# Optimization experiments

Hardware: AMD Instinct MI355X
Metric: run time of the kernel (lower is better)

## Reference

```python
import jax, jax.numpy as jnp
import numpy as np

B, N_ATOMS = 8192, 64      # molecules, atoms per molecule
DIM, EXTRA, N_CLS = 70, 7, 11
N_FP = 10000               # fingerprint vocab


def setup_inputs() -> dict:
    key = jax.random.key(0)
    ks = jax.random.split(key, 9)
    atoms = jax.random.randint(ks[0], (B, N_ATOMS), 0, N_FP, dtype=jnp.int64 if jax.config.jax_enable_x64 else jnp.int32)
    adjacency = jax.random.uniform(ks[1], (B, N_ATOMS, N_ATOMS), dtype=jnp.float32)
    sel_desc = jax.random.normal(ks[2], (B, EXTRA), dtype=jnp.float32)
    embed_table = jax.random.normal(ks[3], (N_FP, DIM), dtype=jnp.float32)
    w1 = jax.random.normal(ks[4], (DIM, DIM), dtype=jnp.float32) * 0.05
    b1 = jax.random.normal(ks[5], (DIM,), dtype=jnp.float32) * 0.05
    w2 = jax.random.normal(ks[6], (DIM, DIM), dtype=jnp.float32) * 0.05
    b2 = jax.random.normal(ks[7], (DIM,), dtype=jnp.float32) * 0.05
    wp = jax.random.normal(ks[8], (DIM + EXTRA, N_CLS), dtype=jnp.float32) * 0.05
    bp = jnp.zeros((N_CLS,), dtype=jnp.float32)
    return {"atoms": atoms, "adjacency": adjacency, "sel_desc": sel_desc,
            "embed_table": embed_table, "w1": w1, "b1": b1,
            "w2": w2, "b2": b2, "wp": wp, "bp": bp}


def reference(atoms, adjacency, sel_desc, embed_table, w1, b1, w2, b2, wp, bp):
    # embed atoms: [B, n, dim]
    x = embed_table[atoms]
    # message-passing layers: relu(linear) then (block-diagonal == batched) adjacency matmul
    for w, b in ((w1, b1), (w2, b2)):
        h = jax.nn.relu(jnp.einsum('bnd,de->bne', x, w) + b)
        x = jnp.einsum('bnm,bmd->bnd', adjacency, h)
    # segment-sum pool over atoms per molecule (sum_axis)
    y = jnp.sum(x, axis=1)                       # [B, dim]
    y = jnp.concatenate([y, sel_desc], axis=1)   # [B, dim+extra]
    return jnp.einsum('bd,dc->bc', y, wp) + bp   # [B, 11]
```

## Files before the change

kernel.cpp:

```cpp
#include <hip/hip_runtime.h>
#include <hip/hip_bf16.h>

#define NFP   10000
#define DIM   70
#define DPAD  72
#define NATOMS 64

typedef short  short8  __attribute__((ext_vector_type(8)));
typedef float  floatx4 __attribute__((ext_vector_type(4)));

__device__ inline unsigned short f2bf(float f) {
  union { float f; unsigned u; } x; x.f = f;
  unsigned r = x.u + 0x7fffu + ((x.u >> 16) & 1u);
  return (unsigned short)(r >> 16);
}

__device__ inline ushort2 pk2bf(float a, float b) {
  __hip_bfloat162 h = __float22bfloat162_rn(make_float2(a, b));
  union { __hip_bfloat162 h; ushort2 u; } c; c.h = h; return c.u;
}

__global__ __launch_bounds__(256) void precompute_G(
    const float* __restrict__ emb, const float* __restrict__ w1,
    const float* __restrict__ b1,  const float* __restrict__ w2,
    unsigned short* __restrict__ G) {
  __shared__ float w1s[DIM * DPAD];
  __shared__ float w2s[DIM * DPAD];
  __shared__ float b1s[DPAD];
  __shared__ float embs[32 * DPAD];
  __shared__ float e1s[32 * DPAD];
  const int t = threadIdx.x;

  for (int i = t; i < DIM * DPAD; i += 256) {
    int r = i / DPAD, c = i % DPAD;
    float v1 = 0.f, v2 = 0.f;
    if (c < DIM) { v1 = w1[r * DIM + c]; v2 = w2[r * DIM + c]; }
    w1s[i] = v1; w2s[i] = v2;
  }
  if (t < DPAD) b1s[t] = (t < DIM) ? b1[t] : 0.f;
  const int row0 = blockIdx.x * 32;
  for (int i = t; i < 32 * DPAD; i += 256) {
    int r = i / DPAD, c = i % DPAD;
    int vr = row0 + r;
    embs[i] = (vr < NFP && c < DIM) ? emb[vr * DIM + c] : 0.f;
  }
  __syncthreads();

  for (int task = t; task < 32 * 18; task += 256) {
    int r = task / 18, c4 = (task % 18) * 4;
    float4 acc = *(const float4*)&b1s[c4];
    for (int k = 0; k < DIM; k++) {
      float e = embs[r * DPAD + k];
      float4 w = *(const float4*)&w1s[k * DPAD + c4];
      acc.x = fmaf(e, w.x, acc.x); acc.y = fmaf(e, w.y, acc.y);
      acc.z = fmaf(e, w.z, acc.z); acc.w = fmaf(e, w.w, acc.w);
    }
    acc.x = fmaxf(acc.x, 0.f); acc.y = fmaxf(acc.y, 0.f);
    acc.z = fmaxf(acc.z, 0.f); acc.w = fmaxf(acc.w, 0.f);
    *(float4*)&e1s[r * DPAD + c4] = acc;
  }
  __syncthreads();

  for (int task = t; task < 32 * 18; task += 256) {
    int r = task / 18, c4 = (task % 18) * 4;
    int vr = row0 + r;
    if (vr >= NFP) continue;
    float ax = 0.f, ay = 0.f, az = 0.f, aw = 0.f;
    for (int k = 0; k < DIM; k++) {
      float e = e1s[r * DPAD + k];
      float4 w = *(const float4*)&w2s[k * DPAD + c4];
      ax = fmaf(e, w.x, ax); ay = fmaf(e, w.y, ay);
      az = fmaf(e, w.z, az); aw = fmaf(e, w.w, aw);
    }
    unsigned short* gp = G + vr * DPAD + c4;
    gp[0] = f2bf(ax); gp[1] = f2bf(ay); gp[2] = f2bf(az); gp[3] = f2bf(aw);
  }
}

__global__ __launch_bounds__(256) void mol_fused(
    const int* __restrict__ atoms, const float* __restrict__ adj,
    const float* __restrict__ b2,  const unsigned short* __restrict__ G,
    float* __restrict__ yws) {
  __shared__ unsigned short adjs[64 * DPAD];
  __shared__ unsigned short gTs[80 * DPAD];
  __shared__ float cwave[4 * 64];
  __shared__ float cvec[64];
  __shared__ float b2p[80];
  __shared__ float yacc[4 * 80];
  __shared__ int   satoms[64];

  const int b = blockIdx.x;
  const int t = threadIdx.x;
  const int w = t >> 6, lane = t & 63;
  const int q = lane >> 4, li = lane & 15;

  if (t < 64) satoms[t] = atoms[b * 64 + t];
  if (t < 80) b2p[t] = (t < DIM) ? b2[t] : 0.f;
  __syncthreads();

  {
    const float* ap = adj + (size_t)b * 4096;
    const int mc = (t & 15) * 4;
    const int a  = t >> 4;
    float4 cs = make_float4(0.f, 0.f, 0.f, 0.f);
#pragma unroll
    for (int it = 0; it < 4; it++) {
      int n = a + 16 * it;
      float4 v = *(const float4*)(ap + n * 64 + mc);
      cs.x += v.x; cs.y += v.y; cs.z += v.z; cs.w += v.w;
      ushort2 lo = pk2bf(v.x, v.y);
      ushort2 hi = pk2bf(v.z, v.w);
      ushort4 u; u.x = lo.x; u.y = lo.y; u.z = hi.x; u.w = hi.y;
      *(ushort4*)&adjs[n * DPAD + mc] = u;
    }
#pragma unroll
    for (int s = 16; s <= 32; s <<= 1) {
      cs.x += __shfl_xor(cs.x, s); cs.y += __shfl_xor(cs.y, s);
      cs.z += __shfl_xor(cs.z, s); cs.w += __shfl_xor(cs.w, s);
    }
    if (((t >> 4) & 3) == 0) *(float4*)&cwave[w * 64 + mc] = cs;
  }

  {
    const int m = t & 63;
    const int row = satoms[m];
    const uint4* Gv = (const uint4*)G;
    for (int ch = w; ch < 9; ch += 4) {
      uint4 v = Gv[row * 9 + ch];
      unsigned short* gp = &gTs[(ch * 8) * DPAD + m];
      gp[0 * DPAD] = (unsigned short)(v.x & 0xffff);
      gp[1 * DPAD] = (unsigned short)(v.x >> 16);
      gp[2 * DPAD] = (unsigned short)(v.y & 0xffff);
      gp[3 * DPAD] = (unsigned short)(v.y >> 16);
      gp[4 * DPAD] = (unsigned short)(v.z & 0xffff);
      gp[5 * DPAD] = (unsigned short)(v.z >> 16);
      gp[6 * DPAD] = (unsigned short)(v.w & 0xffff);
      gp[7 * DPAD] = (unsigned short)(v.w >> 16);
    }
    for (int i = t; i < 8 * DPAD; i += 256) gTs[72 * DPAD + i] = 0;
  }
  __syncthreads();

  if (t < 64) {
    cvec[t] = cwave[t] + cwave[64 + t] + cwave[128 + t] + cwave[192 + t];
  }

  const int R = w * 16;
  short8 a0 = *(const short8*)&adjs[(R + li) * DPAD + q * 8];
  short8 a1 = *(const short8*)&adjs[(R + li) * DPAD + 32 + q * 8];
  floatx4 acc[5];
#pragma unroll
  for (int nt = 0; nt < 5; nt++) {
    floatx4 z = {0.f, 0.f, 0.f, 0.f};
    short8 b0 = *(const short8*)&gTs[(nt * 16 + li) * DPAD + q * 8];
    short8 b1 = *(const short8*)&gTs[(nt * 16 + li) * DPAD + 32 + q * 8];
    z = __builtin_amdgcn_mfma_f32_16x16x32_bf16(a0, b0, z, 0, 0, 0);
    z = __builtin_amdgcn_mfma_f32_16x16x32_bf16(a1, b1, z, 0, 0, 0);
    acc[nt] = z;
  }
  __syncthreads();

  float ps[5];
#pragma unroll
  for (int nt = 0; nt < 5; nt++) {
    int d = nt * 16 + li;
    float bb = b2p[d];
    float p = 0.f;
#pragma unroll
    for (int r = 0; r < 4; r++) {
      float h = fmaxf(acc[nt][r] + bb, 0.f);
      p = fmaf(cvec[R + q * 4 + r], h, p);
    }
    p += __shfl_xor(p, 16);
    p += __shfl_xor(p, 32);
    ps[nt] = p;
  }
  if (q == 0) {
#pragma unroll
    for (int nt = 0; nt < 5; nt++) yacc[w * 80 + nt * 16 + li] = ps[nt];
  }
  __syncthreads();

  if (t < DIM) {
    float s = yacc[t] + yacc[80 + t] + yacc[160 + t] + yacc[240 + t];
    yws[(size_t)b * DIM + t] = s;
  }
}

__global__ __launch_bounds__(256) void proj_out(
    const float* __restrict__ yws, const float* __restrict__ sel,
    const float* __restrict__ wp,  const float* __restrict__ bp,
    float* __restrict__ out, int B) {
  __shared__ float wps[77 * 11];
  __shared__ float bps[11];
  const int t = threadIdx.x;
  for (int i = t; i < 77 * 11; i += 256) wps[i] = wp[i];
  if (t < 11) bps[t] = bp[t];
  __syncthreads();
  const int gid = blockIdx.x * 256 + t;
  if (gid >= B * 11) return;
  const int b = gid / 11, c = gid % 11;
  float s = bps[c];
  const float* yp = yws + (size_t)b * DIM;
#pragma unroll 7
  for (int d = 0; d < DIM; d++) s = fmaf(yp[d], wps[d * 11 + c], s);
  const float* sp = sel + (size_t)b * 7;
#pragma unroll
  for (int d = 0; d < 7; d++) s = fmaf(sp[d], wps[(DIM + d) * 11 + c], s);
  out[gid] = s;
}

extern "C" void kernel_launch(void* const* d_in, const int* in_sizes, int n_in,
                              void* d_out, int out_size, void* d_ws, size_t ws_size,
                              hipStream_t stream) {
  const int*   atoms = (const int*)d_in[0];
  const float* adj   = (const float*)d_in[1];
  const float* sel   = (const float*)d_in[2];
  const float* emb   = (const float*)d_in[3];
  const float* w1    = (const float*)d_in[4];
  const float* b1    = (const float*)d_in[5];
  const float* w2    = (const float*)d_in[6];
  const float* b2    = (const float*)d_in[7];
  const float* wp    = (const float*)d_in[8];
  const float* bp    = (const float*)d_in[9];

  const int B = in_sizes[0] / NATOMS;
  unsigned short* G = (unsigned short*)d_ws;
  float* yws = (float*)((char*)d_ws + (2 << 20));

  precompute_G<<<(NFP + 31) / 32, 256, 0, stream>>>(emb, w1, b1, w2, G);
  mol_fused<<<B, 256, 0, stream>>>(atoms, adj, b2, G, yws);
  proj_out<<<(B * 11 + 255) / 256, 256, 0, stream>>>(yws, sel, wp, bp, (float*)d_out, B);
}
```

Measured before the change: 255.1 us.

## Fuse output projection into molecule kernel and load adjacency directly into MFMA registers

Folds the final projection into the per-molecule kernel, so the intermediate pooled vector is no longer written to workspace and a third launch is gone. Adjacency is now read straight from global memory into bf16 MFMA A-fragments, skipping the shared-memory staging, and column sums are formed with wave shuffles. The gathered G rows are written as packed 32-bit pairs and one barrier is dropped. Each block now reloads the 77x11 projection weights, and the occupancy hint of 6 may limit registers.

```diff
diff --git a/kernel.cpp b/kernel.cpp
--- a/kernel.cpp
+++ b/kernel.cpp
@@ -3,7 +3,7 @@
 
 #define NFP   10000
 #define DIM   70
-#define DPAD  72
+#define GPAD  72
 #define NATOMS 64
 
 typedef short  short8  __attribute__((ext_vector_type(8)));
@@ -24,23 +24,23 @@
     const float* __restrict__ emb, const float* __restrict__ w1,
     const float* __restrict__ b1,  const float* __restrict__ w2,
     unsigned short* __restrict__ G) {
-  __shared__ float w1s[DIM * DPAD];
-  __shared__ float w2s[DIM * DPAD];
-  __shared__ float b1s[DPAD];
-  __shared__ float embs[32 * DPAD];
-  __shared__ float e1s[32 * DPAD];
+  __shared__ float w1s[DIM * GPAD];
+  __shared__ float w2s[DIM * GPAD];
+  __shared__ float b1s[GPAD];
+  __shared__ float embs[32 * GPAD];
+  __shared__ float e1s[32 * GPAD];
   const int t = threadIdx.x;
 
-  for (int i = t; i < DIM * DPAD; i += 256) {
-    int r = i / DPAD, c = i % DPAD;
+  for (int i = t; i < DIM * GPAD; i += 256) {
+    int r = i / GPAD, c = i % GPAD;
     float v1 = 0.f, v2 = 0.f;
     if (c < DIM) { v1 = w1[r * DIM + c]; v2 = w2[r * DIM + c]; }
     w1s[i] = v1; w2s[i] = v2;
   }
-  if (t < DPAD) b1s[t] = (t < DIM) ? b1[t] : 0.f;
+  if (t < GPAD) b1s[t] = (t < DIM) ? b1[t] : 0.f;
   const int row0 = blockIdx.x * 32;
-  for (int i = t; i < 32 * DPAD; i += 256) {
-    int r = i / DPAD, c = i % DPAD;
+  for (int i = t; i < 32 * GPAD; i += 256) {
+    int r = i / GPAD, c = i % GPAD;
     int vr = row0 + r;
     embs[i] = (vr < NFP && c < DIM) ? emb[vr * DIM + c] : 0.f;
   }
@@ -50,14 +50,14 @@
     int r = task / 18, c4 = (task % 18) * 4;
     float4 acc = *(const float4*)&b1s[c4];
     for (int k = 0; k < DIM; k++) {
-      float e = embs[r * DPAD + k];
-      float4 w = *(const float4*)&w1s[k * DPAD + c4];
+      float e = embs[r * GPAD + k];
+      float4 w = *(const float4*)&w1s[k * GPAD + c4];
       acc.x = fmaf(e, w.x, acc.x); acc.y = fmaf(e, w.y, acc.y);
       acc.z = fmaf(e, w.z, acc.z); acc.w = fmaf(e, w.w, acc.w);
     }
     acc.x = fmaxf(acc.x, 0.f); acc.y = fmaxf(acc.y, 0.f);
     acc.z = fmaxf(acc.z, 0.f); acc.w = fmaxf(acc.w, 0.f);
-    *(float4*)&e1s[r * DPAD + c4] = acc;
+    *(float4*)&e1s[r * GPAD + c4] = acc;
   }
   __syncthreads();
 
@@ -67,110 +67,120 @@
     if (vr >= NFP) continue;
     float ax = 0.f, ay = 0.f, az = 0.f, aw = 0.f;
     for (int k = 0; k < DIM; k++) {
-      float e = e1s[r * DPAD + k];
-      float4 w = *(const float4*)&w2s[k * DPAD + c4];
+      float e = e1s[r * GPAD + k];
+      float4 w = *(const float4*)&w2s[k * GPAD + c4];
       ax = fmaf(e, w.x, ax); ay = fmaf(e, w.y, ay);
       az = fmaf(e, w.z, az); aw = fmaf(e, w.w, aw);
     }
-    unsigned short* gp = G + vr * DPAD + c4;
+    unsigned short* gp = G + vr * GPAD + c4;
     gp[0] = f2bf(ax); gp[1] = f2bf(ay); gp[2] = f2bf(az); gp[3] = f2bf(aw);
   }
 }
 
-__global__ __launch_bounds__(256) void mol_fused(
+__global__ __launch_bounds__(256, 6) void mol_fused(
     const int* __restrict__ atoms, const float* __restrict__ adj,
-    const float* __restrict__ b2,  const unsigned short* __restrict__ G,
-    float* __restrict__ yws) {
-  __shared__ unsigned short adjs[64 * DPAD];
-  __shared__ unsigned short gTs[80 * DPAD];
-  __shared__ float cwave[4 * 64];
-  __shared__ float cvec[64];
+    const float* __restrict__ sel, const float* __restrict__ b2,
+    const float* __restrict__ wp,  const float* __restrict__ bp,
+    const unsigned short* __restrict__ G, float* __restrict__ out) {
+  __shared__ unsigned short gTs[80 * GPAD];
+  __shared__ float cpart[4 * 64];
   __shared__ float b2p[80];
+  __shared__ float wps[77 * 11];
+  __shared__ float bps[11];
   __shared__ float yacc[4 * 80];
-  __shared__ int   satoms[64];
+  __shared__ float yv[80];
 
   const int b = blockIdx.x;
   const int t = threadIdx.x;
   const int w = t >> 6, lane = t & 63;
   const int q = lane >> 4, li = lane & 15;
-
-  if (t < 64) satoms[t] = atoms[b * 64 + t];
+  const int R = w * 16;
+
+  const float* rp = adj + (size_t)b * 4096 + (R + li) * 64;
+  float4 v0 = *(const float4*)(rp + q * 8);
+  float4 v1 = *(const float4*)(rp + q * 8 + 4);
+  float4 v2 = *(const float4*)(rp + 32 + q * 8);
+  float4 v3 = *(const float4*)(rp + 36 + q * 8);
+  union { short8 s; ushort2 u[4]; } A0, A1;
+  A0.u[0] = pk2bf(v0.x, v0.y); A0.u[1] = pk2bf(v0.z, v0.w);
+  A0.u[2] = pk2bf(v1.x, v1.y); A0.u[3] = pk2bf(v1.z, v1.w);
+  A1.u[0] = pk2bf(v2.x, v2.y); A1.u[1] = pk2bf(v2.z, v2.w);
+  A1.u[2] = pk2bf(v3.x, v3.y); A1.u[3] = pk2bf(v3.z, v3.w);
+  {
+    float c[16] = {v0.x, v0.y, v0.z, v0.w, v1.x, v1.y, v1.z, v1.w,
+                   v2.x, v2.y, v2.z, v2.w, v3.x, v3.y, v3.z, v3.w};
+#pragma unroll
+    for (int m = 1; m <= 8; m <<= 1)
+#pragma unroll
+      for (int i = 0; i < 16; i++) c[i] += __shfl_xor(c[i], m);
+    if (li == 0) {
+      float* cp = &cpart[w * 64];
+      *(float4*)&cp[q * 8]      = make_float4(c[0], c[1], c[2], c[3]);
+      *(float4*)&cp[q * 8 + 4]  = make_float4(c[4], c[5], c[6], c[7]);
+      *(float4*)&cp[32 + q * 8]     = make_float4(c[8],  c[9],  c[10], c[11]);
+      *(float4*)&cp[32 + q * 8 + 4] = make_float4(c[12], c[13], c[14], c[15]);
+    }
+  }
+
+  for (int i = t; i < 77 * 11; i += 256) wps[i] = wp[i];
+  if (t < 11) bps[t] = bp[t];
   if (t < 80) b2p[t] = (t < DIM) ? b2[t] : 0.f;
-  __syncthreads();
 
   {
-    const float* ap = adj + (size_t)b * 4096;
-    const int mc = (t & 15) * 4;
-    const int a  = t >> 4;
-    float4 cs = make_float4(0.f, 0.f, 0.f, 0.f);
-#pragma unroll
-    for (int it = 0; it < 4; it++) {
-      int n = a + 16 * it;
-      float4 v = *(const float4*)(ap + n * 64 + mc);
-      cs.x += v.x; cs.y += v.y; cs.z += v.z; cs.w += v.w;
-      ushort2 lo = pk2bf(v.x, v.y);
-      ushort2 hi = pk2bf(v.z, v.w);
-      ushort4 u; u.x = lo.x; u.y = lo.y; u.z = hi.x; u.w = hi.y;
-      *(ushort4*)&adjs[n * DPAD + mc] = u;
-    }
-#pragma unroll
-    for (int s = 16; s <= 32; s <<= 1) {
-      cs.x += __shfl_xor(cs.x, s); cs.y += __shfl_xor(cs.y, s);
-      cs.z += __shfl_xor(cs.z, s); cs.w += __shfl_xor(cs.w, s);
-    }
-    if (((t >> 4) & 3) == 0) *(float4*)&cwave[w * 64 + mc] = cs;
-  }
-
-  {
-    const int m = t & 63;
-    const int row = satoms[m];
     const uint4* Gv = (const uint4*)G;
-    for (int ch = w; ch < 9; ch += 4) {
-      uint4 v = Gv[row * 9 + ch];
-      unsigned short* gp = &gTs[(ch * 8) * DPAD + m];
-      gp[0 * DPAD] = (unsigned short)(v.x & 0xffff);
-      gp[1 * DPAD] = (unsigned short)(v.x >> 16);
-      gp[2 * DPAD] = (unsigned short)(v.y & 0xffff);
-      gp[3 * DPAD] = (unsigned short)(v.y >> 16);
-      gp[4 * DPAD] = (unsigned short)(v.z & 0xffff);
-      gp[5 * DPAD] = (unsigned short)(v.z >> 16);
-      gp[6 * DPAD] = (unsigned short)(v.w & 0xffff);
-      gp[7 * DPAD] = (unsigned short)(v.w >> 16);
-    }
-    for (int i = t; i < 8 * DPAD; i += 256) gTs[72 * DPAD + i] = 0;
-  }
-  __syncthreads();
-
-  if (t < 64) {
-    cvec[t] = cwave[t] + cwave[64 + t] + cwave[128 + t] + cwave[192 + t];
-  }
-
-  const int R = w * 16;
-  short8 a0 = *(const short8*)&adjs[(R + li) * DPAD + q * 8];
-  short8 a1 = *(const short8*)&adjs[(R + li) * DPAD + 32 + q * 8];
+    const int p = t & 31;
+    int2 aidx = *(const int2*)(atoms + b * 64 + 2 * p);
+    int ch = t >> 5;
+#pragma unroll
+    for (int pass = 0; pass < 2; pass++) {
+      if (pass == 1) { if (t >= 32) break; ch = 8; }
+      uint4 g0 = Gv[(unsigned)aidx.x * 9 + ch];
+      uint4 g1 = Gv[(unsigned)aidx.y * 9 + ch];
+      unsigned base = (unsigned)(ch * 8) * GPAD + 2 * p;
+      unsigned* d0 = (unsigned*)&gTs[base];
+      d0[0 * (GPAD / 2) * 0] = 0;
+      *(unsigned*)&gTs[base + 0 * GPAD] = (g0.x & 0xffffu) | (g1.x << 16);
+      *(unsigned*)&gTs[base + 1 * GPAD] = (g0.x >> 16) | (g1.x & 0xffff0000u);
+      *(unsigned*)&gTs[base + 2 * GPAD] = (g0.y & 0xffffu) | (g1.y << 16);
+      *(unsigned*)&gTs[base + 3 * GPAD] = (g0.y >> 16) | (g1.y & 0xffff0000u);
+      *(unsigned*)&gTs[base + 4 * GPAD] = (g0.z & 0xffffu) | (g1.z << 16);
+      *(unsigned*)&gTs[base + 5 * GPAD] = (g0.z >> 16) | (g1.z & 0xffff0000u);
+      *(unsigned*)&gTs[base + 6 * GPAD] = (g0.w & 0xffffu) | (g1.w << 16);
+      *(unsigned*)&gTs[base + 7 * GPAD] = (g0.w >> 16) | (g1.w & 0xffff0000u);
+    }
+  }
+  if (t < 72) {
+    uint4 zz; zz.x = zz.y = zz.z = zz.w = 0u;
+    *(uint4*)&gTs[72 * GPAD + t * 8] = zz;
+  }
+  __syncthreads();
+
+  float cr[4];
+#pragma unroll
+  for (int r = 0; r < 4; r++) {
+    int m = R + q * 4 + r;
+    cr[r] = cpart[m] + cpart[64 + m] + cpart[128 + m] + cpart[192 + m];
+  }
+
   floatx4 acc[5];
 #pragma unroll
   for (int nt = 0; nt < 5; nt++) {
     floatx4 z = {0.f, 0.f, 0.f, 0.f};
-    short8 b0 = *(const short8*)&gTs[(nt * 16 + li) * DPAD + q * 8];
-    short8 b1 = *(const short8*)&gTs[(nt * 16 + li) * DPAD + 32 + q * 8];
-    z = __builtin_amdgcn_mfma_f32_16x16x32_bf16(a0, b0, z, 0, 0, 0);
-    z = __builtin_amdgcn_mfma_f32_16x16x32_bf16(a1, b1, z, 0, 0, 0);
+    short8 b0 = *(const short8*)&gTs[(nt * 16 + li) * GPAD + q * 8];
+    short8 b1 = *(const short8*)&gTs[(nt * 16 + li) * GPAD + 32 + q * 8];
+    z = __builtin_amdgcn_mfma_f32_16x16x32_bf16(A0.s, b0, z, 0, 0, 0);
+    z = __builtin_amdgcn_mfma_f32_16x16x32_bf16(A1.s, b1, z, 0, 0, 0);
     acc[nt] = z;
   }
-  __syncthreads();
 
   float ps[5];
 #pragma unroll
   for (int nt = 0; nt < 5; nt++) {
-    int d = nt * 16 + li;
-    float bb = b2p[d];
+    float bb = b2p[nt * 16 + li];
     float p = 0.f;
 #pragma unroll
-    for (int r = 0; r < 4; r++) {
-      float h = fmaxf(acc[nt][r] + bb, 0.f);
-      p = fmaf(cvec[R + q * 4 + r], h, p);
-    }
+    for (int r = 0; r < 4; r++)
+      p = fmaf(cr[r], fmaxf(acc[nt][r] + bb, 0.f), p);
     p += __shfl_xor(p, 16);
     p += __shfl_xor(p, 32);
     ps[nt] = p;
@@ -181,33 +191,20 @@
   }
   __syncthreads();
 
-  if (t < DIM) {
-    float s = yacc[t] + yacc[80 + t] + yacc[160 + t] + yacc[240 + t];
-    yws[(size_t)b * DIM + t] = s;
-  }
-}
-
-__global__ __launch_bounds__(256) void proj_out(
-    const float* __restrict__ yws, const float* __restrict__ sel,
-    const float* __restrict__ wp,  const float* __restrict__ bp,
-    float* __restrict__ out, int B) {
-  __shared__ float wps[77 * 11];
-  __shared__ float bps[11];
-  const int t = threadIdx.x;
-  for (int i = t; i < 77 * 11; i += 256) wps[i] = wp[i];
-  if (t < 11) bps[t] = bp[t];
-  __syncthreads();
-  const int gid = blockIdx.x * 256 + t;
-  if (gid >= B * 11) return;
-  const int b = gid / 11, c = gid % 11;
-  float s = bps[c];
-  const float* yp = yws + (size_t)b * DIM;
+  if (t < 77) {
+    float s;
+    if (t < DIM) s = yacc[t] + yacc[80 + t] + yacc[160 + t] + yacc[240 + t];
+    else         s = sel[(size_t)b * 7 + (t - DIM)];
+    yv[t] = s;
+  }
+  __syncthreads();
+
+  if (t < 11) {
+    float s = bps[t];
 #pragma unroll 7
-  for (int d = 0; d < DIM; d++) s = fmaf(yp[d], wps[d * 11 + c], s);
-  const float* sp = sel + (size_t)b * 7;
-#pragma unroll
-  for (int d = 0; d < 7; d++) s = fmaf(sp[d], wps[(DIM + d) * 11 + c], s);
-  out[gid] = s;
+    for (int d = 0; d < 77; d++) s = fmaf(yv[d], wps[d * 11 + t], s);
+    out[(size_t)b * 11 + t] = s;
+  }
 }
 
 extern "C" void kernel_launch(void* const* d_in, const int* in_sizes, int n_in,
@@ -226,9 +223,7 @@
 
   const int B = in_sizes[0] / NATOMS;
   unsigned short* G = (unsigned short*)d_ws;
-  float* yws = (float*)((char*)d_ws + (2 << 20));
 
   precompute_G<<<(NFP + 31) / 32, 256, 0, stream>>>(emb, w1, b1, w2, G);
-  mol_fused<<<B, 256, 0, stream>>>(atoms, adj, b2, G, yws);
-  proj_out<<<(B * 11 + 255) / 256, 256, 0, stream>>>(yws, sel, wp, bp, (float*)d_out, B);
-}
+  mol_fused<<<B, 256, 0, stream>>>(atoms, adj, sel, b2, wp, bp, G, (float*)d_out);
+}
```

Result: no change. 260.0 us (+1.9%).
